# Kernel tuning notes

Measured on AMD Instinct MI355X. Metric: run time of the kernel, lower is better.

Reference implementation:

```python
import jax, jax.numpy as jnp
import numpy as np

# ---- static circuit configuration (matches module init) ----
C = 6        # Fock cutoff (strawberryfields.tf cutoff_dim)
N = 5        # modes / wires
OUTPUT = 2   # output_size
LAYERS = 4   # layers
M = N * (N - 1) + max(1, N - 1)  # 24: params per interferometer

# ladder operators in truncated Fock basis
_a = np.diag(np.sqrt(np.arange(1, C)), 1)
A = jnp.asarray(_a, dtype=jnp.complex64)          # annihilation
AD = A.conj().T                                    # creation
NUM = jnp.arange(C, dtype=jnp.float32)             # number operator diag
I1 = jnp.eye(C, dtype=jnp.complex64)
A1 = jnp.kron(A, I1)   # a on mode 1 of a 2-mode block
A2 = jnp.kron(I1, A)   # a on mode 2 of a 2-mode block


def _expm(H, order=16, s=6):
    # scaling-and-squaring + Horner Taylor; fully differentiable, small matrices only
    Hs = H * jnp.asarray(1.0 / (2 ** s), H.dtype)
    I = jnp.eye(H.shape[-1], dtype=H.dtype)
    R = I
    for k in range(order, 0, -1):
        R = I + (Hs @ R) * jnp.asarray(1.0 / k, H.dtype)
    for _ in range(s):
        R = R @ R
    return R


def disp_gate(r, phi):
    al = jax.lax.complex(r * jnp.cos(phi), r * jnp.sin(phi))
    return _expm(al * AD - jnp.conj(al) * A)


def squeeze_gate(r):
    # S(r, 0) = exp(r/2 (a^2 - adag^2))
    return _expm(jax.lax.complex(r, jnp.zeros_like(r)) * 0.5 * (A @ A - AD @ AD))


def rot_gate(phi):
    return jnp.diag(jnp.exp(1j * phi * NUM))


def kerr_gate(kap):
    return jnp.diag(jnp.exp(1j * kap * NUM * NUM))


def bs_gate(theta, phi):
    ep = jnp.exp(1j * phi)
    H = ep * (A1 @ A2.conj().T) - jnp.conj(ep) * (A1.conj().T @ A2)
    th = jax.lax.complex(theta, jnp.zeros_like(theta))
    return _expm(th * H).reshape(C, C, C, C)


def apply1(U, psi, m):
    psi = jnp.tensordot(U, psi, axes=([1], [m]))
    return jnp.moveaxis(psi, 0, m)


def apply2(U4, psi, m):
    # U4[o1,o2,i1,i2] acting on adjacent modes (m, m+1)
    psi = jnp.tensordot(U4, psi, axes=([2, 3], [m, m + 1]))
    return jnp.moveaxis(psi, [0, 1], [m, m + 1])


def interferometer(p, psi):
    T = N * (N - 1) // 2
    theta, phi, rphi = p[:T], p[T:2 * T], p[-(N - 1):]
    n = 0
    for l in range(N):
        for k in range(N - 1):
            if (l + k) % 2 == 0:  # same condition as (l+k)%2 != 1 being False
                psi = apply2(bs_gate(theta[n], phi[n]), psi, k)
                n += 1
    for i in range(max(1, N - 1)):
        psi = apply1(rot_gate(rphi[i]), psi, i)
    return psi


def linear_layer(p, psi):
    psi = interferometer(p[:M], psi)
    for i in range(N):
        psi = apply1(squeeze_gate(p[M + i]), psi, i)
    psi = interferometer(p[M + N:2 * M + N], psi)
    dr = p[2 * M + N:2 * M + 2 * N]
    dp = p[2 * M + 2 * N:2 * M + 3 * N]
    for i in range(N):
        psi = apply1(disp_gate(dr[i], dp[i]), psi, i)
    return psi


def circuit(xi, lin, act, last_act):
    psi = jnp.zeros((C,) * N, jnp.complex64).at[(0,) * N].set(1.0)
    zero = jnp.float32(0.0)
    for i in range(N):  # Displacement encoding of input
        psi = apply1(disp_gate(xi[i], zero), psi, i)
    for l in range(LAYERS - 1):
        psi = linear_layer(lin[l], psi)
        for i in range(N):  # Kerr activation
            psi = apply1(kerr_gate(act[l, i]), psi, i)
    psi = linear_layer(lin[LAYERS - 1], psi)
    for i in range(OUTPUT):  # last activation on first OUTPUT modes
        psi = apply1(kerr_gate(last_act[i]), psi, i)
    X = A + AD  # x quadrature, hbar=2 (StrawberryFields convention)
    return jnp.stack([jnp.real(jnp.vdot(psi, apply1(X, psi, i))) for i in range(OUTPUT)])


def setup_inputs() -> dict:
    key = jax.random.key(0)
    k1, k2, k3, k4 = jax.random.split(key, 4)
    B = 2048
    x = jax.random.uniform(k1, (B, N), dtype=jnp.float32)
    linear_params = 0.001 * jax.random.normal(k2, (LAYERS, 2 * M + 3 * N), dtype=jnp.float32)
    activation_params = 0.001 * jax.random.normal(k3, (LAYERS - 1, N), dtype=jnp.float32)
    last_activation_params = 0.001 * jax.random.normal(k4, (N,), dtype=jnp.float32)
    return {
        "x": x,
        "linear_params": linear_params,
        "activation_params": activation_params,
        "last_activation_params": last_activation_params,
    }


def reference(x, linear_params, activation_params, last_activation_params):
    f = lambda xi: circuit(xi, linear_params, activation_params, last_activation_params)
    return jax.vmap(f)(x)  # [B, OUTPUT]
```

## Files before the change

### kernel.cpp

```cpp
#include <hip/hip_runtime.h>


typedef float    vf2 __attribute__((ext_vector_type(2)));
typedef _Float16 h2  __attribute__((ext_vector_type(2)));
typedef _Float16 h4  __attribute__((ext_vector_type(4)));

__device__ __forceinline__ h2 pkfma(const h2 a, const h2 b, const h2 c) {
    return __builtin_elementwise_fma(a, b, c);
}

__device__ __forceinline__ void cmadd(float &ax, float &ay, const float2 u, const float2 v) {
    ax = fmaf(u.x, v.x, ax);
    ax = fmaf(-u.y, v.y, ax);
    ay = fmaf(u.x, v.y, ay);
    ay = fmaf(u.y, v.x, ay);
}

constexpr int BS_SN[11]  = {1,2,3,4,5,6,5,4,3,2,1};
constexpr int BS_OFF[11] = {0,1,5,14,30,55,91,116,132,141,145};

__device__ const int d_BS_OFF[12] = {0,1,5,14,30,55,91,116,132,141,145,146};
__device__ const int d_BS_SN[11]  = {1,2,3,4,5,6,5,4,3,2,1};

__global__ void gates_kernel(const float* __restrict__ lin,
                             const float* __restrict__ act,
                             const float* __restrict__ lact,
                             h2* __restrict__ bsh,
                             h2* __restrict__ sgh)
{
    __shared__ float2 B0[1296];
    __shared__ float2 B1[1296];
    const int tid = threadIdx.x;

    if (blockIdx.x < 80) {
        const int g = blockIdx.x;
        const int l = g / 20;
        const int w = g % 20;
        const int q = w / 10;
        const int n = w % 10;
        const float theta = lin[l*63 + (q ? 29 : 0) + n];
        const float phi   = lin[l*63 + (q ? 39 : 10) + n];
        const float ts = theta * 0.015625f;
        const float cp = cosf(phi), sp = sinf(phi);
        const float2 u  = make_float2( ts*cp, ts*sp);
        const float2 w2 = make_float2(-ts*cp, ts*sp);

        float2 *R = B0, *T = B1;
        for (int e = tid; e < 1296; e += 256)
            R[e] = make_float2((e % 37 == 0) ? 1.f : 0.f, 0.f);
        __syncthreads();

        for (int k = 16; k >= 1; --k) {
            const float invk = 1.f / (float)k;
            for (int e = tid; e < 1296; e += 256) {
                const int row = e / 36, c = e - row*36;
                const int i = row / 6, j = row - (row/6)*6;
                float ax = 0.f, ay = 0.f;
                if (i < 5 && j > 0) {
                    const float coef = sqrtf((float)((i+1)*j));
                    const float2 x = R[(row+5)*36 + c];
                    const float px = u.x*x.x - u.y*x.y;
                    const float py = u.x*x.y + u.y*x.x;
                    ax = fmaf(coef, px, ax); ay = fmaf(coef, py, ay);
                }
                if (i > 0 && j < 5) {
                    const float coef = sqrtf((float)(i*(j+1)));
                    const float2 x = R[(row-5)*36 + c];
                    const float px = w2.x*x.x - w2.y*x.y;
                    const float py = w2.x*x.y + w2.y*x.x;
                    ax = fmaf(coef, px, ax); ay = fmaf(coef, py, ay);
                }
                T[e] = make_float2(((row == c) ? 1.f : 0.f) + ax*invk, ay*invk);
            }
            __syncthreads();
            float2* tmp = R; R = T; T = tmp;
        }
        for (int s2 = 0; s2 < 6; ++s2) {
            for (int e = tid; e < 1296; e += 256) {
                const int row = e / 36, c = e - row*36;
                float ax = 0.f, ay = 0.f;
                #pragma unroll 6
                for (int k = 0; k < 36; ++k)
                    cmadd(ax, ay, R[row*36 + k], R[k*36 + c]);
                T[e] = make_float2(ax, ay);
            }
            __syncthreads();
            float2* tmp = R; R = T; T = tmp;
        }
        for (int idx = tid; idx < 146; idx += 256) {
            int nn = 0;
            while (idx >= d_BS_OFF[nn+1]) ++nn;
            const int sn  = d_BS_SN[nn];
            const int rel = idx - d_BS_OFF[nn];
            const int p = rel / sn, qq = rel % sn;
            const int imin = (nn > 5) ? (nn - 5) : 0;
            const int row = 5*(imin + p)  + nn;
            const int col = 5*(imin + qq) + nn;
            const float2 z = R[row*36 + col];
            bsh[g*292 + 2*idx    ] = (h2){(_Float16)z.x, (_Float16)z.x};
            bsh[g*292 + 2*idx + 1] = (h2){(_Float16)z.y, (_Float16)z.y};
        }
    } else {
        const int t = tid;
        if (t >= 40) return;
        const int l  = t / 10;
        const int gi = t % 10;
        float2 G[36];
        if (gi < 5) {
            const int m = gi;
            const float r    = lin[l*63 + 24 + m];
            const float rphi = (m < 4) ? lin[l*63 + 20 + m] : 0.f;
            float R[36], T[36];
            #pragma unroll
            for (int e = 0; e < 36; ++e) R[e] = (e % 7 == 0) ? 1.f : 0.f;
            float hp[4];
            #pragma unroll
            for (int i = 0; i < 4; ++i)
                hp[i] = 0.5f * r * sqrtf((float)((i+1)*(i+2))) * 0.015625f;
            for (int k = 16; k >= 1; --k) {
                const float invk = 1.f / (float)k;
                #pragma unroll
                for (int i = 0; i < 6; ++i) {
                    #pragma unroll
                    for (int c = 0; c < 6; ++c) {
                        float a = 0.f;
                        if (i < 4)  a = fmaf( hp[i],   R[(i+2)*6 + c], a);
                        if (i >= 2) a = fmaf(-hp[i-2], R[(i-2)*6 + c], a);
                        T[i*6+c] = ((i == c) ? 1.f : 0.f) + a*invk;
                    }
                }
                #pragma unroll
                for (int e = 0; e < 36; ++e) R[e] = T[e];
            }
            for (int s2 = 0; s2 < 6; ++s2) {
                #pragma unroll
                for (int i = 0; i < 6; ++i) {
                    #pragma unroll
                    for (int c = 0; c < 6; ++c) {
                        float a = 0.f;
                        #pragma unroll
                        for (int k = 0; k < 6; ++k) a = fmaf(R[i*6+k], R[k*6+c], a);
                        T[i*6+c] = a;
                    }
                }
                #pragma unroll
                for (int e = 0; e < 36; ++e) R[e] = T[e];
            }
            #pragma unroll
            for (int c = 0; c < 6; ++c) {
                const float cc = cosf(rphi * (float)c), ss = sinf(rphi * (float)c);
                #pragma unroll
                for (int o = 0; o < 6; ++o)
                    G[o*6 + c] = make_float2(R[o*6+c]*cc, R[o*6+c]*ss);
            }
        } else {
            const int m = gi - 5;
            const float dr   = lin[l*63 + 53 + m];
            const float dp   = lin[l*63 + 58 + m];
            const float rphi = (m < 4) ? lin[l*63 + 49 + m] : 0.f;
            const float kap  = (l < 3) ? act[l*5 + m] : ((m < 2) ? lact[m] : 0.f);
            const float2 al = make_float2(dr * cosf(dp), dr * sinf(dp));
            float2 R[36], T[36];
            #pragma unroll
            for (int e = 0; e < 36; ++e)
                R[e] = make_float2((e % 7 == 0) ? 1.f : 0.f, 0.f);
            float2 cm[6], cpb[6];
            #pragma unroll
            for (int i = 0; i < 6; ++i) {
                const float sm  = sqrtf((float)i)     * 0.015625f;
                const float sp2 = sqrtf((float)(i+1)) * 0.015625f;
                cm[i]  = make_float2( al.x*sm,  al.y*sm);
                cpb[i] = make_float2(-al.x*sp2, al.y*sp2);
            }
            for (int k = 16; k >= 1; --k) {
                const float invk = 1.f / (float)k;
                #pragma unroll
                for (int i = 0; i < 6; ++i) {
                    #pragma unroll
                    for (int c = 0; c < 6; ++c) {
                        float ax = 0.f, ay = 0.f;
                        if (i >= 1) cmadd(ax, ay, cm[i],  R[(i-1)*6 + c]);
                        if (i < 5)  cmadd(ax, ay, cpb[i], R[(i+1)*6 + c]);
                        T[i*6+c] = make_float2(((i == c) ? 1.f : 0.f) + ax*invk, ay*invk);
                    }
                }
                #pragma unroll
                for (int e = 0; e < 36; ++e) R[e] = T[e];
            }
            for (int s2 = 0; s2 < 6; ++s2) {
                #pragma unroll
                for (int i = 0; i < 6; ++i) {
                    #pragma unroll
                    for (int c = 0; c < 6; ++c) {
                        float ax = 0.f, ay = 0.f;
                        #pragma unroll
                        for (int k = 0; k < 6; ++k) cmadd(ax, ay, R[i*6+k], R[k*6+c]);
                        T[i*6+c] = make_float2(ax, ay);
                    }
                }
                #pragma unroll
                for (int e = 0; e < 36; ++e) R[e] = T[e];
            }
            #pragma unroll
            for (int o = 0; o < 6; ++o) {
                const float ko = kap * (float)(o*o);
                const float2 kp = make_float2(cosf(ko), sinf(ko));
                #pragma unroll
                for (int c = 0; c < 6; ++c) {
                    const float rc = rphi * (float)c;
                    const float2 rp = make_float2(cosf(rc), sinf(rc));
                    const float2 z = R[o*6 + c];
                    const float2 t1 = make_float2(kp.x*z.x - kp.y*z.y, kp.x*z.y + kp.y*z.x);
                    G[o*6 + c] = make_float2(t1.x*rp.x - t1.y*rp.y, t1.x*rp.y + t1.y*rp.x);
                }
            }
        }
        h2* outp = sgh + (l*10 + gi)*72;
        #pragma unroll
        for (int e = 0; e < 36; ++e) {
            outp[2*e    ] = (h2){(_Float16)G[e].x, (_Float16)G[e].x};
            outp[2*e + 1] = (h2){(_Float16)G[e].y, (_Float16)G[e].y};
        }
    }
}

__global__ void dcol_kernel(const float* __restrict__ x,
                            float* __restrict__ dcol, const int total)
{
    const int i = blockIdx.x * 256 + threadIdx.x;
    if (i >= total) return;
    const float xv = x[i];
    float a[5];
    #pragma unroll
    for (int j = 0; j < 5; ++j) a[j] = xv * sqrtf((float)(j+1)) * 0.015625f;
    float R[36], T[36];
    #pragma unroll
    for (int e = 0; e < 36; ++e) R[e] = (e % 7 == 0) ? 1.f : 0.f;
    for (int k = 16; k >= 1; --k) {
        const float invk = 1.f / (float)k;
        #pragma unroll
        for (int r = 0; r < 6; ++r) {
            #pragma unroll
            for (int c = 0; c < 6; ++c) {
                float acc = 0.f;
                if (r >= 1) acc = fmaf( a[r-1], R[(r-1)*6 + c], acc);
                if (r < 5)  acc = fmaf(-a[r],   R[(r+1)*6 + c], acc);
                T[r*6+c] = ((r == c) ? 1.f : 0.f) + acc*invk;
            }
        }
        #pragma unroll
        for (int e = 0; e < 36; ++e) R[e] = T[e];
    }
    for (int s2 = 0; s2 < 6; ++s2) {
        #pragma unroll
        for (int r = 0; r < 6; ++r) {
            #pragma unroll
            for (int c = 0; c < 6; ++c) {
                float acc = 0.f;
                #pragma unroll
                for (int k = 0; k < 6; ++k) acc = fmaf(R[r*6+k], R[k*6+c], acc);
                T[r*6+c] = acc;
            }
        }
        #pragma unroll
        for (int e = 0; e < 36; ++e) R[e] = T[e];
    }
    #pragma unroll
    for (int j = 0; j < 6; ++j) dcol[i*6 + j] = R[j*6 + 0];
}


template<int SA, int SB, int n, int R0, int R1>
__device__ __forceinline__ void bs_rows(const h2* __restrict__ U,
                                        h4* __restrict__ psi,
                                        const int base, const bool act)
{
    constexpr int sn = BS_SN[n], uoff = BS_OFF[n];
    constexpr int imin = (n > 5) ? (n - 5) : 0;
    if (!act) return;
    h2 vR[sn], vI[sn];
    #pragma unroll
    for (int q = 0; q < sn; ++q) {
        const int c = 5*(imin + q) + n;
        const h4 v = psi[base + (c/6)*SA + (c%6)*SB];
        vR[q] = (h2){v.x, v.y};
        vI[q] = (h2){v.z, v.w};
    }
    h2 oR[R1-R0], oI[R1-R0];
    #pragma unroll
    for (int p = R0; p < R1; ++p) {
        const h2* Up = U + 2*(uoff + p*sn);
        h2 ur = Up[0], ui = Up[1];
        h2 aR = ur * vR[0];
        aR = pkfma(-ui, vI[0], aR);
        h2 aI = ur * vI[0];
        aI = pkfma(ui, vR[0], aI);
        #pragma unroll
        for (int q = 1; q < sn; ++q) {
            ur = Up[2*q]; ui = Up[2*q + 1];
            aR = pkfma(ur, vR[q], aR);
            aR = pkfma(-ui, vI[q], aR);
            aI = pkfma(ur, vI[q], aI);
            aI = pkfma(ui, vR[q], aI);
        }
        oR[p-R0] = aR; oI[p-R0] = aI;
    }
    #pragma unroll
    for (int p = R0; p < R1; ++p) {
        const int c = 5*(imin + p) + n;
        const h2 r = oR[p-R0], m = oI[p-R0];
        psi[base + (c/6)*SA + (c%6)*SB] = (h4){r.x, r.y, m.x, m.y};
    }
}

template<int SA, int SB>
__device__ __forceinline__ void pass_bs(const h2* __restrict__ U,
                                        h4* __restrict__ psi,
                                        const int base, const bool act, const int qid)
{
    if (qid == 0) {
        bs_rows<SA,SB,5,0,6>(U, psi, base, act);
    } else if (qid == 1) {
        bs_rows<SA,SB,4,0,5>(U, psi, base, act);
        bs_rows<SA,SB,2,0,3>(U, psi, base, act);
        bs_rows<SA,SB,1,0,2>(U, psi, base, act);
    } else if (qid == 2) {
        bs_rows<SA,SB,6,0,5>(U, psi, base, act);
        bs_rows<SA,SB,8,0,3>(U, psi, base, act);
        bs_rows<SA,SB,9,0,2>(U, psi, base, act);
    } else {
        bs_rows<SA,SB,3,0,4>(U, psi, base, act);
        bs_rows<SA,SB,7,0,4>(U, psi, base, act);
        bs_rows<SA,SB,0,0,1>(U, psi, base, act);
        bs_rows<SA,SB,10,0,1>(U, psi, base, act);
    }
    __syncthreads();
}

template<int SM, bool SP>
__device__ __forceinline__ void sg_fiber(const h2* __restrict__ G,
                                         h4* __restrict__ psi,
                                         const int base)
{
    h2 vR[6], vI[6];
    #pragma unroll
    for (int k = 0; k < 6; ++k) {
        const h4 v = psi[base + k*SM];
        vR[k] = (h2){v.x, v.y};
        vI[k] = (h2){v.z, v.w};
    }
    h2 oR[6], oI[6];
    #pragma unroll
    for (int o = 0; o < 6; ++o) {
        const int k0 = SP ? (o & 1) : 0;
        const int st = SP ? 2 : 1;
        h2 ur = G[2*(o*6 + k0)], ui = G[2*(o*6 + k0) + 1];
        h2 aR = ur * vR[k0];
        aR = pkfma(-ui, vI[k0], aR);
        h2 aI = ur * vI[k0];
        aI = pkfma(ui, vR[k0], aI);
        #pragma unroll
        for (int k = k0 + st; k < 6; k += st) {
            ur = G[2*(o*6 + k)]; ui = G[2*(o*6 + k) + 1];
            aR = pkfma(ur, vR[k], aR);
            aR = pkfma(-ui, vI[k], aR);
            aI = pkfma(ur, vI[k], aI);
            aI = pkfma(ui, vR[k], aI);
        }
        oR[o] = aR; oI[o] = aI;
    }
    #pragma unroll
    for (int o = 0; o < 6; ++o)
        psi[base + o*SM] = (h4){oR[o].x, oR[o].y, oI[o].x, oI[o].y};
}

template<int SM, int S0, int S1, int S2, int S3, bool SP>
__device__ __forceinline__ void pass_sg(const h2* __restrict__ G,
                                        h4* __restrict__ psi,
                                        const int4 dg0, const int4 dg1, const bool act1)
{
    {
        const int base = dg0.x*S0 + dg0.y*S1 + dg0.z*S2 + dg0.w*S3;
        sg_fiber<SM,SP>(G, psi, base);
    }
    if (act1) {
        const int base = dg1.x*S0 + dg1.y*S1 + dg1.z*S2 + dg1.w*S3;
        sg_fiber<SM,SP>(G, psi, base);
    }
    __syncthreads();
}

__global__ __launch_bounds__(1024, 8)
void qnet_kernel(const h2* __restrict__ bs,
                 const h2* __restrict__ sg,
                 const float* __restrict__ dcol,
                 float* __restrict__ out,
                 const int B)
{
    __shared__ __align__(16) h4 psi[7992];
    __shared__ float stf[60];
    __shared__ float red[64];
    __shared__ float2 ps01[2][36];
    __shared__ float2 ps23[2][36];
    __shared__ float2 f234[2][216];

    const int tid = threadIdx.x;
    const int b   = blockIdx.x;

    const int lim = B * 30;
    if (tid < 60) stf[tid] = (b*60 + tid < lim) ? dcol[b*60 + tid] : 0.f;
    __syncthreads();

    if (tid < 144) {
        const int part = tid / 36;
        const int idx  = tid - part*36;
        const int p    = part & 1;
        const bool m01 = part < 2;
        const int i = idx / 6, j = idx - (idx/6)*6;
        const int n = i + j;
        const int imin = (n > 5) ? (n - 5) : 0;
        const int sn   = d_BS_SN[n];
        const int prow = i - imin;
        const h2* U = bs + (m01 ? 0 : 1)*292 + 2*(d_BS_OFF[n] + prow*sn);
        const float* dA = stf + p*30 + (m01 ? 0 : 12);
        const float* dB = dA + 6;
        float ar = 0.f, ai = 0.f;
        for (int q = 0; q < sn; ++q) {
            const float ur = (float)U[2*q].x, ui = (float)U[2*q+1].x;
            const float dd = dA[imin+q] * dB[n-imin-q];
            ar = fmaf(ur, dd, ar); ai = fmaf(ui, dd, ai);
        }
        if (m01) ps01[p][idx] = make_float2(ar, ai);
        else     ps23[p][idx] = make_float2(ar, ai);
    }
    __syncthreads();

    if (tid < 432) {
        const int p  = tid / 216;
        const int r  = tid - p*216;
        const int i2 = r / 36, i34 = r - i2*36;
        const int i3 = i34 / 6, i4 = i34 - i3*6;
        const int n  = i3 + i4;
        const int imin = (n > 5) ? (n - 5) : 0;
        const int sn   = d_BS_SN[n];
        const int prow = i3 - imin;
        const h2* U = bs + 3*292 + 2*(d_BS_OFF[n] + prow*sn);
        const float* d4 = stf + p*30 + 24;
        float ar = 0.f, ai = 0.f;
        for (int q = 0; q < sn; ++q) {
            const float ur = (float)U[2*q].x, ui = (float)U[2*q+1].x;
            const float2 w23 = ps23[p][i2*6 + (imin+q)];
            const float dd = d4[n-imin-q];
            ar = fmaf(dd, ur*w23.x - ui*w23.y, ar);
            ai = fmaf(dd, ur*w23.y + ui*w23.x, ai);
        }
        f234[p][r] = make_float2(ar, ai);
    }
    __syncthreads();

    for (int e = tid; e < 7776; e += 1024) {
        int t = e;
        const int i4 = t % 6; t /= 6;
        const int i3 = t % 6; t /= 6;
        const int i2 = t % 6; t /= 6;
        const int i1 = t % 6; t /= 6;
        const int i0 = t;
        const int addr = 6*i0 + i1 + 36*i2 + 221*i3 + 1334*i4;
        const int i01 = i0*6 + i1;
        const int r   = i2*36 + i3*6 + i4;
        const float2 a0 = ps01[0][i01], b0 = f234[0][r];
        const float2 a1 = ps01[1][i01], b1 = f234[1][r];
        const float v0r = a0.x*b0.x - a0.y*b0.y, v0i = a0.x*b0.y + a0.y*b0.x;
        const float v1r = a1.x*b1.x - a1.y*b1.y, v1i = a1.x*b1.y + a1.y*b1.x;
        psi[addr] = (h4){(_Float16)v0r, (_Float16)v1r, (_Float16)v0i, (_Float16)v1i};
    }
    __syncthreads();

    const int sub = tid & 255;
    const int qid = __builtin_amdgcn_readfirstlane(tid >> 8);
    const bool act = sub < 216;
    const int f = act ? sub : 215;
    const int fa = f / 36, rem = f - fa*36;
    const int fb = rem / 6, fc = rem - fb*6;
    const int baseK0 = fa*36 + fb*221 + fc*1334;
    const int baseK1 = fa*6  + fb*221 + fc*1334;
    const int baseK2 = rem   + fa*1334;
    const int baseK3 = f;

    int4 dg0, dg1;
    { int t = tid;        dg0.x = t % 6; t /= 6; dg0.y = t % 6; t /= 6; dg0.z = t % 6; dg0.w = t / 6; }
    { int t = tid + 1024; dg1.x = t % 6; t /= 6; dg1.y = t % 6; t /= 6; dg1.z = t % 6; dg1.w = t / 6; }
    const bool act1 = tid < 272;

    for (int l = 0; l < 4; ++l) {
        const h2* bsl = bs + l * 20 * 292;
        const h2* sgl = sg + l * 10 * 72;
        for (int hf = 0; hf < 2; ++hf) {
            const h2* bh = bsl + hf * 10 * 292;
            const h2* sh = sgl + hf * 5 * 72;
            const bool first = (l == 0) && (hf == 0);
            const bool last = (l == 3) && (hf == 1);
            if (!first) {
                pass_bs<6,1>     (bh + 0*292, psi, baseK0, act, qid);
                pass_bs<36,221>  (bh + 1*292, psi, baseK2, act, qid);
            }
            pass_bs<1,36>    (bh + 2*292, psi, baseK1, act, qid);
            if (!first)
                pass_bs<221,1334>(bh + 3*292, psi, baseK3, act, qid);
            pass_bs<6,1>     (bh + 4*292, psi, baseK0, act, qid);
            pass_bs<36,221>  (bh + 5*292, psi, baseK2, act, qid);
            pass_bs<1,36>    (bh + 6*292, psi, baseK1, act, qid);
            if (!last)
                pass_bs<221,1334>(bh + 7*292, psi, baseK3, act, qid);
            pass_bs<6,1>     (bh + 8*292, psi, baseK0, act, qid);
            if (!last)
                pass_bs<36,221>  (bh + 9*292, psi, baseK2, act, qid);
            if (hf == 0) {
                pass_sg<6,    1,36,221,1334, true>(sh + 0*72, psi, dg0, dg1, act1);
                pass_sg<1,    6,36,221,1334, true>(sh + 1*72, psi, dg0, dg1, act1);
                pass_sg<36,   1,6,221,1334,  true>(sh + 2*72, psi, dg0, dg1, act1);
                pass_sg<221,  1,6,36,1334,   true>(sh + 3*72, psi, dg0, dg1, act1);
                pass_sg<1334, 1,6,36,221,    true>(sh + 4*72, psi, dg0, dg1, act1);
            } else {
                pass_sg<6,    1,36,221,1334, false>(sh + 0*72, psi, dg0, dg1, act1);
                pass_sg<1,    6,36,221,1334, false>(sh + 1*72, psi, dg0, dg1, act1);
                if (!last) {
                    pass_sg<36,   1,6,221,1334,  false>(sh + 2*72, psi, dg0, dg1, act1);
                    pass_sg<221,  1,6,36,1334,   false>(sh + 3*72, psi, dg0, dg1, act1);
                    pass_sg<1334, 1,6,36,221,    false>(sh + 4*72, psi, dg0, dg1, act1);
                }
            }
        }
    }

    float s0a = 0.f, s0b = 0.f, s1a = 0.f, s1b = 0.f;
    for (int fr = tid; fr < 1296; fr += 1024) {
        const int q0 = fr % 6;
        const int q1 = (fr / 6) % 6;
        const int q2 = (fr / 36) % 6;
        const int q3 = fr / 216;
        const int base0 = q0*1 + q1*36 + q2*221 + q3*1334;
        #pragma unroll
        for (int j = 0; j < 5; ++j) {
            const h4 a = psi[base0 + 6*j];
            const h4 c = psi[base0 + 6*(j+1)];
            const float w = sqrtf((float)(j+1));
            s0a = fmaf(w, fmaf((float)a.z, (float)c.z, (float)a.x*(float)c.x), s0a);
            s0b = fmaf(w, fmaf((float)a.w, (float)c.w, (float)a.y*(float)c.y), s0b);
        }
        const int base1 = q0*6 + q1*36 + q2*221 + q3*1334;
        #pragma unroll
        for (int j = 0; j < 5; ++j) {
            const h4 a = psi[base1 + j];
            const h4 c = psi[base1 + j + 1];
            const float w = sqrtf((float)(j+1));
            s1a = fmaf(w, fmaf((float)a.z, (float)c.z, (float)a.x*(float)c.x), s1a);
            s1b = fmaf(w, fmaf((float)a.w, (float)c.w, (float)a.y*(float)c.y), s1b);
        }
    }
    #pragma unroll
    for (int off = 32; off > 0; off >>= 1) {
        s0a += __shfl_down(s0a, off, 64);
        s0b += __shfl_down(s0b, off, 64);
        s1a += __shfl_down(s1a, off, 64);
        s1b += __shfl_down(s1b, off, 64);
    }
    if ((tid & 63) == 0) {
        const int w = tid >> 6;
        red[w*4 + 0] = s0a; red[w*4 + 1] = s1a;
        red[w*4 + 2] = s0b; red[w*4 + 3] = s1b;
    }
    __syncthreads();
    if (tid == 0) {
        float r0 = 0.f, r1 = 0.f, r2 = 0.f, r3 = 0.f;
        #pragma unroll
        for (int w = 0; w < 16; ++w) {
            r0 += red[w*4 + 0]; r1 += red[w*4 + 1];
            r2 += red[w*4 + 2]; r3 += red[w*4 + 3];
        }
        const int b0 = 2*b, b1 = 2*b + 1;
        out[b0*2 + 0] = 2.f * r0;
        out[b0*2 + 1] = 2.f * r1;
        if (b1 < B) {
            out[b1*2 + 0] = 2.f * r2;
            out[b1*2 + 1] = 2.f * r3;
        }
    }
}

extern "C" void kernel_launch(void* const* d_in, const int* in_sizes, int n_in,
                              void* d_out, int out_size, void* d_ws, size_t ws_size,
                              hipStream_t stream)
{
    const float* x    = (const float*)d_in[0];
    const float* lin  = (const float*)d_in[1];
    const float* act  = (const float*)d_in[2];
    const float* lact = (const float*)d_in[3];
    float* out = (float*)d_out;

    const int B = in_sizes[0] / 5;

    h2*    bsh = (h2*)d_ws;
    h2*    sgh = bsh + 80*292;
    float* dc  = (float*)(sgh + 40*72);

    gates_kernel<<<dim3(81), dim3(256), 0, stream>>>(lin, act, lact, bsh, sgh);
    const int total = B * 5;
    dcol_kernel<<<dim3((total + 255)/256), dim3(256), 0, stream>>>(x, dc, total);
    qnet_kernel<<<dim3((B + 1) / 2), dim3(1024), 0, stream>>>(bsh, sgh, dc, out, B);
}
```

Before: 771.4 us.

## Merge gate and displacement prep kernels and cut expm Taylor/squaring cost

Folds the displacement-column kernel into the gate-preparation kernel, so one launch replaces two. The scaling-and-squaring exponentials drop from order 16 with 6 squarings to order 10 with 2 squarings. The displacement gate now computes only the first column with a matrix-vector Taylor series of order 30, instead of the full matrix. This cuts launch overhead and prep arithmetic, at some risk to accuracy for larger parameters.

New measurement: 712.2 us (median of 2 runs). 7.7% less time.

```diff
diff --git a/kernel.cpp b/kernel.cpp
--- a/kernel.cpp
+++ b/kernel.cpp
@@ -22,11 +22,14 @@
 __device__ const int d_BS_OFF[12] = {0,1,5,14,30,55,91,116,132,141,145,146};
 __device__ const int d_BS_SN[11]  = {1,2,3,4,5,6,5,4,3,2,1};
 
-__global__ void gates_kernel(const float* __restrict__ lin,
-                             const float* __restrict__ act,
-                             const float* __restrict__ lact,
-                             h2* __restrict__ bsh,
-                             h2* __restrict__ sgh)
+__global__ void prep_kernel(const float* __restrict__ lin,
+                            const float* __restrict__ act,
+                            const float* __restrict__ lact,
+                            const float* __restrict__ x,
+                            h2* __restrict__ bsh,
+                            h2* __restrict__ sgh,
+                            float* __restrict__ dcol,
+                            const int total)
 {
     __shared__ float2 B0[1296];
     __shared__ float2 B1[1296];
@@ -40,7 +43,7 @@
         const int n = w % 10;
         const float theta = lin[l*63 + (q ? 29 : 0) + n];
         const float phi   = lin[l*63 + (q ? 39 : 10) + n];
-        const float ts = theta * 0.015625f;
+        const float ts = theta * 0.25f;
         const float cp = cosf(phi), sp = sinf(phi);
         const float2 u  = make_float2( ts*cp, ts*sp);
         const float2 w2 = make_float2(-ts*cp, ts*sp);
@@ -50,7 +53,7 @@
             R[e] = make_float2((e % 37 == 0) ? 1.f : 0.f, 0.f);
         __syncthreads();
 
-        for (int k = 16; k >= 1; --k) {
+        for (int k = 10; k >= 1; --k) {
             const float invk = 1.f / (float)k;
             for (int e = tid; e < 1296; e += 256) {
                 const int row = e / 36, c = e - row*36;
@@ -58,16 +61,16 @@
                 float ax = 0.f, ay = 0.f;
                 if (i < 5 && j > 0) {
                     const float coef = sqrtf((float)((i+1)*j));
-                    const float2 x = R[(row+5)*36 + c];
-                    const float px = u.x*x.x - u.y*x.y;
-                    const float py = u.x*x.y + u.y*x.x;
+                    const float2 xv = R[(row+5)*36 + c];
+                    const float px = u.x*xv.x - u.y*xv.y;
+                    const float py = u.x*xv.y + u.y*xv.x;
                     ax = fmaf(coef, px, ax); ay = fmaf(coef, py, ay);
                 }
                 if (i > 0 && j < 5) {
                     const float coef = sqrtf((float)(i*(j+1)));
-                    const float2 x = R[(row-5)*36 + c];
-                    const float px = w2.x*x.x - w2.y*x.y;
-                    const float py = w2.x*x.y + w2.y*x.x;
+                    const float2 xv = R[(row-5)*36 + c];
+                    const float px = w2.x*xv.x - w2.y*xv.y;
+                    const float py = w2.x*xv.y + w2.y*xv.x;
                     ax = fmaf(coef, px, ax); ay = fmaf(coef, py, ay);
                 }
                 T[e] = make_float2(((row == c) ? 1.f : 0.f) + ax*invk, ay*invk);
@@ -75,7 +78,7 @@
             __syncthreads();
             float2* tmp = R; R = T; T = tmp;
         }
-        for (int s2 = 0; s2 < 6; ++s2) {
+        for (int s2 = 0; s2 < 2; ++s2) {
             for (int e = tid; e < 1296; e += 256) {
                 const int row = e / 36, c = e - row*36;
                 float ax = 0.f, ay = 0.f;
@@ -100,7 +103,7 @@
             bsh[g*292 + 2*idx    ] = (h2){(_Float16)z.x, (_Float16)z.x};
             bsh[g*292 + 2*idx + 1] = (h2){(_Float16)z.y, (_Float16)z.y};
         }
-    } else {
+    } else if (blockIdx.x == 80) {
         const int t = tid;
         if (t >= 40) return;
         const int l  = t / 10;
@@ -116,8 +119,8 @@
             float hp[4];
             #pragma unroll
             for (int i = 0; i < 4; ++i)
-                hp[i] = 0.5f * r * sqrtf((float)((i+1)*(i+2))) * 0.015625f;
-            for (int k = 16; k >= 1; --k) {
+                hp[i] = 0.5f * r * sqrtf((float)((i+1)*(i+2))) * 0.25f;
+            for (int k = 10; k >= 1; --k) {
                 const float invk = 1.f / (float)k;
                 #pragma unroll
                 for (int i = 0; i < 6; ++i) {
@@ -132,7 +135,7 @@
                 #pragma unroll
                 for (int e = 0; e < 36; ++e) R[e] = T[e];
             }
-            for (int s2 = 0; s2 < 6; ++s2) {
+            for (int s2 = 0; s2 < 2; ++s2) {
                 #pragma unroll
                 for (int i = 0; i < 6; ++i) {
                     #pragma unroll
@@ -167,12 +170,12 @@
             float2 cm[6], cpb[6];
             #pragma unroll
             for (int i = 0; i < 6; ++i) {
-                const float sm  = sqrtf((float)i)     * 0.015625f;
-                const float sp2 = sqrtf((float)(i+1)) * 0.015625f;
+                const float sm  = sqrtf((float)i)     * 0.25f;
+                const float sp2 = sqrtf((float)(i+1)) * 0.25f;
                 cm[i]  = make_float2( al.x*sm,  al.y*sm);
                 cpb[i] = make_float2(-al.x*sp2, al.y*sp2);
             }
-            for (int k = 16; k >= 1; --k) {
+            for (int k = 10; k >= 1; --k) {
                 const float invk = 1.f / (float)k;
                 #pragma unroll
                 for (int i = 0; i < 6; ++i) {
@@ -187,7 +190,7 @@
                 #pragma unroll
                 for (int e = 0; e < 36; ++e) R[e] = T[e];
             }
-            for (int s2 = 0; s2 < 6; ++s2) {
+            for (int s2 = 0; s2 < 2; ++s2) {
                 #pragma unroll
                 for (int i = 0; i < 6; ++i) {
                     #pragma unroll
@@ -221,52 +224,32 @@
             outp[2*e    ] = (h2){(_Float16)G[e].x, (_Float16)G[e].x};
             outp[2*e + 1] = (h2){(_Float16)G[e].y, (_Float16)G[e].y};
         }
-    }
-}
-
-__global__ void dcol_kernel(const float* __restrict__ x,
-                            float* __restrict__ dcol, const int total)
-{
-    const int i = blockIdx.x * 256 + threadIdx.x;
-    if (i >= total) return;
-    const float xv = x[i];
-    float a[5];
-    #pragma unroll
-    for (int j = 0; j < 5; ++j) a[j] = xv * sqrtf((float)(j+1)) * 0.015625f;
-    float R[36], T[36];
-    #pragma unroll
-    for (int e = 0; e < 36; ++e) R[e] = (e % 7 == 0) ? 1.f : 0.f;
-    for (int k = 16; k >= 1; --k) {
-        const float invk = 1.f / (float)k;
-        #pragma unroll
-        for (int r = 0; r < 6; ++r) {
-            #pragma unroll
-            for (int c = 0; c < 6; ++c) {
+    } else {
+        const int i = (blockIdx.x - 81) * 256 + tid;
+        if (i >= total) return;
+        const float xv = x[i];
+        float a[5];
+        #pragma unroll
+        for (int j = 0; j < 5; ++j) a[j] = xv * sqrtf((float)(j+1));
+        float w[6];
+        #pragma unroll
+        for (int j = 0; j < 6; ++j) w[j] = (j == 0) ? 1.f : 0.f;
+        for (int k = 30; k >= 1; --k) {
+            const float invk = 1.f / (float)k;
+            float t[6];
+            #pragma unroll
+            for (int r = 0; r < 6; ++r) {
                 float acc = 0.f;
-                if (r >= 1) acc = fmaf( a[r-1], R[(r-1)*6 + c], acc);
-                if (r < 5)  acc = fmaf(-a[r],   R[(r+1)*6 + c], acc);
-                T[r*6+c] = ((r == c) ? 1.f : 0.f) + acc*invk;
-            }
-        }
-        #pragma unroll
-        for (int e = 0; e < 36; ++e) R[e] = T[e];
-    }
-    for (int s2 = 0; s2 < 6; ++s2) {
-        #pragma unroll
-        for (int r = 0; r < 6; ++r) {
-            #pragma unroll
-            for (int c = 0; c < 6; ++c) {
-                float acc = 0.f;
-                #pragma unroll
-                for (int k = 0; k < 6; ++k) acc = fmaf(R[r*6+k], R[k*6+c], acc);
-                T[r*6+c] = acc;
-            }
-        }
-        #pragma unroll
-        for (int e = 0; e < 36; ++e) R[e] = T[e];
-    }
-    #pragma unroll
-    for (int j = 0; j < 6; ++j) dcol[i*6 + j] = R[j*6 + 0];
+                if (r >= 1) acc = fmaf( a[r-1], w[r-1], acc);
+                if (r < 5)  acc = fmaf(-a[r],   w[r+1], acc);
+                t[r] = ((r == 0) ? 1.f : 0.f) + acc*invk;
+            }
+            #pragma unroll
+            for (int j = 0; j < 6; ++j) w[j] = t[j];
+        }
+        #pragma unroll
+        for (int j = 0; j < 6; ++j) dcol[i*6 + j] = w[j];
+    }
 }
 
 
@@ -604,8 +587,8 @@
     h2*    sgh = bsh + 80*292;
     float* dc  = (float*)(sgh + 40*72);
 
-    gates_kernel<<<dim3(81), dim3(256), 0, stream>>>(lin, act, lact, bsh, sgh);
-    const int total = B * 5;
-    dcol_kernel<<<dim3((total + 255)/256), dim3(256), 0, stream>>>(x, dc, total);
+    const int total  = B * 5;
+    const int nprep  = 81 + (total + 255) / 256;
+    prep_kernel<<<dim3(nprep), dim3(256), 0, stream>>>(lin, act, lact, x, bsh, sgh, dc, total);
     qnet_kernel<<<dim3((B + 1) / 2), dim3(1024), 0, stream>>>(bsh, sgh, dc, out, B);
 }
```
